# Kernel optimization log

Hardware: AMD Instinct MI355X
Metric: run time of the kernel (lower is better)

Reference implementation:

```python
import jax, jax.numpy as jnp
import numpy as np

MODES1 = 12
MODES2 = 12
IN_CH = 32
OUT_CH = 32
B, H, W = 16, 256, 256
SCALE = 1.0 / (IN_CH * OUT_CH)


def setup_inputs() -> dict:
    key = jax.random.key(0)
    k1, k2, k3 = jax.random.split(key, 3)
    x = jax.random.normal(k1, (B, IN_CH, H, W), dtype=jnp.float32)
    w1 = SCALE * jax.random.uniform(k2, (IN_CH, OUT_CH, MODES1, MODES2, 2), dtype=jnp.float32)
    w2 = SCALE * jax.random.uniform(k3, (IN_CH, OUT_CH, MODES1, MODES2, 2), dtype=jnp.float32)
    return {"x": x, "weights1": w1, "weights2": w2}


def _compl_mul2d(inp, w):
    # inp: [b,i,x,y] complex ; w: [i,o,x,y,2] real -> complex
    wc = jax.lax.complex(w[..., 0], w[..., 1])
    return jnp.einsum('bixy,ioxy->boxy', inp, wc)


def reference(x, weights1, weights2):
    H_, W_ = x.shape[-2], x.shape[-1]
    m1 = min(MODES1, H_ // 2)
    m2 = min(MODES2, W_ // 2 + 1)
    x_ft = jnp.fft.rfft2(x.astype(jnp.float32))  # [B, Cin, H, W//2+1]
    low = _compl_mul2d(x_ft[:, :, :m1, :m2], weights1[:, :, :m1, :m2])
    high = _compl_mul2d(x_ft[:, :, -m1:, :m2], weights2[:, :, :m1, :m2])
    out_ft = jnp.zeros((x.shape[0], OUT_CH, H_, W_ // 2 + 1), dtype=jnp.complex64)
    out_ft = out_ft.at[:, :, :m1, :m2].set(low)
    out_ft = out_ft.at[:, :, H_ - m1:, :m2].set(high)
    return jnp.fft.irfft2(out_ft, s=(H_, W_)).astype(x.dtype)
```

## Files before the change

### kernel.cpp

```cpp
#include <hip/hip_runtime.h>


#define TPI 6.28318530717958647692f

__global__ __launch_bounds__(256, 2) void k12_hwdft(const float* __restrict__ x,
                                                    float* __restrict__ Xf) {
  __shared__ float2 step2[64];
  __shared__ float red[4 * 13 * 128];
  __shared__ float2 Ys2[13 * 130];
  const int blk = blockIdx.x;
  const int bi = blk >> 1, wh = blk & 1;
  const int t = threadIdx.x;
  const int q = t >> 6, l = t & 63;

  if (t < 64) {
    float s, c;
    sincosf(TPI * (float)t * (1.0f / 256.0f), &s, &c);
    step2[t] = make_float2(c, s);
  }
  __syncthreads();

  const float2* xp2 = reinterpret_cast<const float2*>(x + (size_t)bi * 65536 + wh * 128) + l;
  float2 aC[13], aS12[12];
#pragma unroll
  for (int j = 0; j < 13; j++) aC[j] = make_float2(0.f, 0.f);
#pragma unroll
  for (int j = 0; j < 12; j++) aS12[j] = make_float2(0.f, 0.f);

  const int h0 = q * 16;
#pragma unroll 2
  for (int hh = 0; hh < 16; hh++) {
    int h = h0 + hh;
    float2 x0 = xp2[h * 128];
    float2 x1 = xp2[(h + 64) * 128];
    float2 x2 = xp2[(h + 128) * 128];
    float2 x3 = xp2[(h + 192) * 128];
    float2 p02 = make_float2(x0.x + x2.x, x0.y + x2.y);
    float2 m02 = make_float2(x0.x - x2.x, x0.y - x2.y);
    float2 p13 = make_float2(x1.x + x3.x, x1.y + x3.y);
    float2 m13 = make_float2(x1.x - x3.x, x1.y - x3.y);
    float2 A = make_float2(p02.x + p13.x, p02.y + p13.y);
    float2 Bv = make_float2(p02.x - p13.x, p02.y - p13.y);
    aC[0].x += A.x; aC[0].y += A.y;
    float2 st = step2[h];
    float cj = st.x, sj = st.y;
#pragma unroll
    for (int jj = 0; jj < 12; jj++) {
      const int j = jj + 1, r = j & 3;
      if (r == 0) {
        aC[j].x = fmaf(A.x, cj, aC[j].x);   aC[j].y = fmaf(A.y, cj, aC[j].y);
        aS12[jj].x = fmaf(A.x, sj, aS12[jj].x); aS12[jj].y = fmaf(A.y, sj, aS12[jj].y);
      } else if (r == 2) {
        aC[j].x = fmaf(Bv.x, cj, aC[j].x);  aC[j].y = fmaf(Bv.y, cj, aC[j].y);
        aS12[jj].x = fmaf(Bv.x, sj, aS12[jj].x); aS12[jj].y = fmaf(Bv.y, sj, aS12[jj].y);
      } else if (r == 1) {
        aC[j].x = fmaf(m02.x, cj, fmaf(-m13.x, sj, aC[j].x));
        aC[j].y = fmaf(m02.y, cj, fmaf(-m13.y, sj, aC[j].y));
        aS12[jj].x = fmaf(m02.x, sj, fmaf(m13.x, cj, aS12[jj].x));
        aS12[jj].y = fmaf(m02.y, sj, fmaf(m13.y, cj, aS12[jj].y));
      } else {
        aC[j].x = fmaf(m02.x, cj, fmaf(m13.x, sj, aC[j].x));
        aC[j].y = fmaf(m02.y, cj, fmaf(m13.y, sj, aC[j].y));
        aS12[jj].x = fmaf(m02.x, sj, fmaf(-m13.x, cj, aS12[jj].x));
        aS12[jj].y = fmaf(m02.y, sj, fmaf(-m13.y, cj, aS12[jj].y));
      }
      if (jj < 11) {
        float nc = fmaf(cj, st.x, -(sj * st.y));
        float ns = fmaf(cj, st.y, sj * st.x);
        cj = nc; sj = ns;
      }
    }
  }

  for (int p = 0; p < 2; p++) {
    __syncthreads();
#pragma unroll
    for (int cc = 0; cc < 13; cc++) {
      int cls = p * 13 + cc;
      int j = cls >> 1;
      float2 v;
      if (cls & 1) v = (j == 0) ? make_float2(0.f, 0.f) : aS12[j - 1];
      else v = aC[j];
      *reinterpret_cast<float2*>(&red[(q * 13 + cc) * 128 + 2 * l]) = v;
    }
    __syncthreads();
    for (int idx = t; idx < 13 * 128; idx += 256) {
      int cc = idx >> 7, wl = idx & 127;
      int cls = p * 13 + cc;
      float s = red[(0 * 13 + cc) * 128 + wl] + red[(1 * 13 + cc) * 128 + wl] +
                red[(2 * 13 + cc) * 128 + wl] + red[(3 * 13 + cc) * 128 + wl];
      if (cls & 1) Ys2[(cls >> 1) * 130 + wl].y = s;
      else         Ys2[(cls >> 1) * 130 + wl].x = s;
    }
  }
  __syncthreads();

  if (t < 156) {
    int j = t / 12, kx = t % 12;
    float c1, s1, c2, s2;
    {
      float s, c;
      sincosf(TPI * (float)kx * (1.0f / 256.0f), &s, &c);
      c1 = c; s1 = -s;
      sincosf(TPI * (float)((2 * kx) & 255) * (1.0f / 256.0f), &s, &c);
      c2 = c; s2 = -s;
    }
    const float2* CS = &Ys2[j * 130];
    float pr0 = 1.0f, pi0 = 0.0f;
    float pr1 = c1, pi1 = s1;
    float A = 0, B = 0, D = 0, E = 0;
#pragma unroll 4
    for (int w = 0; w < 128; w += 2) {
      float4 vv = *reinterpret_cast<const float4*>(&CS[w]);
      A = fmaf(vv.x, pr0, A); B = fmaf(vv.x, pi0, B);
      D = fmaf(vv.y, pr0, D); E = fmaf(vv.y, pi0, E);
      A = fmaf(vv.z, pr1, A); B = fmaf(vv.z, pi1, B);
      D = fmaf(vv.w, pr1, D); E = fmaf(vv.w, pi1, E);
      float n0r = pr0 * c2 - pi0 * s2, n0i = pr0 * s2 + pi0 * c2;
      float n1r = pr1 * c2 - pi1 * s2, n1i = pr1 * s2 + pi1 * c2;
      pr0 = n0r; pi0 = n0i; pr1 = n1r; pi1 = n1i;
    }
    float sgn = (wh && (kx & 1)) ? -1.0f : 1.0f;
    A *= sgn; B *= sgn; D *= sgn; E *= sgn;
    float2* Xo = reinterpret_cast<float2*>(Xf) + (size_t)wh * 147456;
    size_t base = (size_t)kx * 512 + bi;
    if (j <= 11) Xo[(size_t)j * 6144 + base] = make_float2(A + E, B - D);
    if (j >= 1)  Xo[(size_t)(24 - j) * 6144 + base] = make_float2(A - E, B + D);
  }
}

__global__ __launch_bounds__(256) void k3_mix(const float* __restrict__ Xf,
                                              const float* __restrict__ w1,
                                              const float* __restrict__ w2,
                                              float* __restrict__ Ff) {
  __shared__ float Xs[1024];
  __shared__ float Ws[2048];
  int m = blockIdx.x;
  int ky = m / 12, kx = m % 12;
  int t = threadIdx.x;
  const float* Xsl = Xf + (size_t)m * 1024;
  for (int e = t; e < 1024; e += 256) Xs[e] = Xsl[e] + Xsl[e + 294912];
  const float* Wp = (ky < 12) ? w1 : w2;
  int myr = (ky < 12) ? ky : ky - 12;
  int woff = myr * 24 + kx * 2;
  for (int e = t; e < 1024; e += 256) {
    float2 wv = *reinterpret_cast<const float2*>(Wp + (size_t)e * 288 + woff);
    Ws[e * 2] = wv.x; Ws[e * 2 + 1] = wv.y;
  }
  __syncthreads();
  int o = t & 31, bh = t >> 5;
  float ar = 0, ai = 0, br = 0, bi_ = 0;
#pragma unroll
  for (int i = 0; i < 32; i++) {
    float wr = Ws[i * 64 + o * 2], wi = Ws[i * 64 + o * 2 + 1];
    float x1r = Xs[bh * 64 + i * 2], x1i = Xs[bh * 64 + i * 2 + 1];
    float x2r = Xs[(bh + 8) * 64 + i * 2], x2i = Xs[(bh + 8) * 64 + i * 2 + 1];
    ar = fmaf(x1r, wr, ar); ar = fmaf(-x1i, wi, ar);
    ai = fmaf(x1r, wi, ai); ai = fmaf(x1i, wr, ai);
    br = fmaf(x2r, wr, br); br = fmaf(-x2i, wi, br);
    bi_ = fmaf(x2r, wi, bi_); bi_ = fmaf(x2i, wr, bi_);
  }
  float scale = (kx == 0 ? 1.0f : 2.0f) * (1.0f / 65536.0f);
  float2* Fo = reinterpret_cast<float2*>(Ff) + (size_t)m * 512;
  Fo[(size_t)bh * 32 + o] = make_float2(ar * scale, ai * scale);
  Fo[(size_t)(bh + 8) * 32 + o] = make_float2(br * scale, bi_ * scale);
}

__global__ __launch_bounds__(256) void k45_inv(const float* __restrict__ Ff,
                                               float* __restrict__ out) {
  __shared__ float tw[128 * 27];
  __shared__ float PQ[13 * 12 * 4];
  __shared__ float Gs[256 * 24];
  const int bo = blockIdx.x;
  const int t = threadIdx.x;
  const int l = t & 63, wq = t >> 6;

  for (int e = t; e < 128 * 13; e += 256) {
    int h = e / 13, j = e % 13;
    float s, c;
    sincosf(TPI * (float)((h * j) & 255) * (1.0f / 256.0f), &s, &c);
    tw[h * 27 + 2 * j] = c;
    tw[h * 27 + 2 * j + 1] = s;
  }
  if (t < 156) {
    int j = t / 12, kx = t % 12;
    const float2* F2 = reinterpret_cast<const float2*>(Ff);
    float lr = 0, li = 0, hr = 0, hi = 0;
    if (j < 12) { float2 v = F2[((size_t)j * 12 + kx) * 512 + bo]; lr = v.x; li = v.y; }
    if (j > 0)  { float2 v = F2[((size_t)(24 - j) * 12 + kx) * 512 + bo]; hr = v.x; hi = v.y; }
    PQ[(j * 12 + kx) * 4 + 0] = lr + hr;
    PQ[(j * 12 + kx) * 4 + 1] = li + hi;
    PQ[(j * 12 + kx) * 4 + 2] = hi - li;
    PQ[(j * 12 + kx) * 4 + 3] = lr - hr;
  }
  __syncthreads();

  if (t < 192) {
    const int kx = t % 12, hq = t / 12;
    float Pr[13], Pi[13], Qr[13], Qi[13];
#pragma unroll
    for (int j = 0; j < 13; j++) {
      Pr[j] = PQ[(j * 12 + kx) * 4 + 0];
      Pi[j] = PQ[(j * 12 + kx) * 4 + 1];
      Qr[j] = PQ[(j * 12 + kx) * 4 + 2];
      Qi[j] = PQ[(j * 12 + kx) * 4 + 3];
    }
    for (int hh = 0; hh < 8; hh++) {
      int h = hh * 16 + hq;
      float Er = 0, Ei = 0, Or = 0, Oi = 0;
#pragma unroll
      for (int j = 0; j < 13; j++) {
        float c = tw[h * 27 + 2 * j], s = tw[h * 27 + 2 * j + 1];
        if (j & 1) {
          Or = fmaf(Pr[j], c, Or); Or = fmaf(Qr[j], s, Or);
          Oi = fmaf(Pi[j], c, Oi); Oi = fmaf(Qi[j], s, Oi);
        } else {
          Er = fmaf(Pr[j], c, Er); Er = fmaf(Qr[j], s, Er);
          Ei = fmaf(Pi[j], c, Ei); Ei = fmaf(Qi[j], s, Ei);
        }
      }
      Gs[h * 24 + 2 * kx] = Er + Or;
      Gs[h * 24 + 2 * kx + 1] = Ei + Oi;
      Gs[(h + 128) * 24 + 2 * kx] = Er - Or;
      Gs[(h + 128) * 24 + 2 * kx + 1] = Ei - Oi;
    }
  }

  float cA[12], sA[12], cB[12], sB[12];
#pragma unroll
  for (int kx = 1; kx < 12; kx++) {
    float s, c;
    __sincosf(TPI * (float)((kx * (2 * l)) & 255) * (1.0f / 256.0f), &s, &c);
    cA[kx] = c; sA[kx] = s;
    __sincosf(TPI * (float)((kx * (2 * l + 1)) & 255) * (1.0f / 256.0f), &s, &c);
    cB[kx] = c; sB[kx] = s;
  }
  __syncthreads();

  float* ob0 = out + ((size_t)bo * 256 + wq * 64) * 256;
  for (int rs = 0; rs < 64; rs++) {
    int rl = wq * 64 + rs;
    float g[24];
    const float4* gr4 = reinterpret_cast<const float4*>(&Gs[rl * 24]);
#pragma unroll
    for (int qq = 0; qq < 6; qq++) {
      float4 v = gr4[qq];
      g[4 * qq] = v.x; g[4 * qq + 1] = v.y; g[4 * qq + 2] = v.z; g[4 * qq + 3] = v.w;
    }
    float E0 = g[0], O0 = 0, E1 = g[0], O1 = 0;
#pragma unroll
    for (int kx = 1; kx < 12; kx++) {
      float ta = g[2 * kx] * cA[kx] - g[2 * kx + 1] * sA[kx];
      float tb = g[2 * kx] * cB[kx] - g[2 * kx + 1] * sB[kx];
      if (kx & 1) { O0 += ta; O1 += tb; } else { E0 += ta; E1 += tb; }
    }
    float* orow = ob0 + rs * 256;
    float2 v0 = make_float2(E0 + O0, E1 + O1);
    float2 v1 = make_float2(E0 - O0, E1 - O1);
    __builtin_nontemporal_store(*reinterpret_cast<double*>(&v0),
                                reinterpret_cast<double*>(&orow[2 * l]));
    __builtin_nontemporal_store(*reinterpret_cast<double*>(&v1),
                                reinterpret_cast<double*>(&orow[128 + 2 * l]));
  }
}

extern "C" void kernel_launch(void* const* d_in, const int* in_sizes, int n_in,
                              void* d_out, int out_size, void* d_ws, size_t ws_size,
                              hipStream_t stream) {
  const float* x = (const float*)d_in[0];
  const float* w1 = (const float*)d_in[1];
  const float* w2 = (const float*)d_in[2];
  float* out = (float*)d_out;
  float* ws = (float*)d_ws;

  float* Xf = ws;
  float* Ff = ws + 589824;

  k12_hwdft<<<1024, 256, 0, stream>>>(x, Xf);
  k3_mix<<<288, 256, 0, stream>>>(Xf, w1, w2, Ff);
  k45_inv<<<512, 256, 0, stream>>>(Ff, out);
}
```

Before: 74.98 us.

## Split forward DFT by H-halves instead of W-halves, removing cross-warp reduction

The forward H/W DFT kernel now gives each block half of the H rows across all 256 columns, one column per thread. Previously each block took half the W columns with four warp groups splitting H. This removes the shared-memory reduction stage and its barriers, and the two partial H sums are added later in the mix kernel. It also software-prefetches the next row's four loads and widens the W-direction DFT to 256 points with four twiddle phases. In exchange it uses scalar loads instead of float2, a longer serial H loop per thread, a larger Ys2 buffer, and more sequential work for the 156 threads in the W stage.

```diff
diff --git a/kernel.cpp b/kernel.cpp
--- a/kernel.cpp
+++ b/kernel.cpp
@@ -6,12 +6,10 @@
 __global__ __launch_bounds__(256, 2) void k12_hwdft(const float* __restrict__ x,
                                                     float* __restrict__ Xf) {
   __shared__ float2 step2[64];
-  __shared__ float red[4 * 13 * 128];
-  __shared__ float2 Ys2[13 * 130];
+  __shared__ float2 Ys2[13 * 260];
   const int blk = blockIdx.x;
-  const int bi = blk >> 1, wh = blk & 1;
+  const int bi = blk >> 1, hf = blk & 1;
   const int t = threadIdx.x;
-  const int q = t >> 6, l = t & 63;
 
   if (t < 64) {
     float s, c;
@@ -20,49 +18,47 @@
   }
   __syncthreads();
 
-  const float2* xp2 = reinterpret_cast<const float2*>(x + (size_t)bi * 65536 + wh * 128) + l;
-  float2 aC[13], aS12[12];
-#pragma unroll
-  for (int j = 0; j < 13; j++) aC[j] = make_float2(0.f, 0.f);
-#pragma unroll
-  for (int j = 0; j < 12; j++) aS12[j] = make_float2(0.f, 0.f);
-
-  const int h0 = q * 16;
-#pragma unroll 2
-  for (int hh = 0; hh < 16; hh++) {
+  const float* xp = x + (size_t)bi * 65536 + t;
+  float aC[13], aS12[12];
+#pragma unroll
+  for (int j = 0; j < 13; j++) aC[j] = 0.0f;
+#pragma unroll
+  for (int j = 0; j < 12; j++) aS12[j] = 0.0f;
+
+  const int h0 = hf * 32;
+  float c0 = xp[h0 * 256];
+  float c1 = xp[(h0 + 64) * 256];
+  float c2 = xp[(h0 + 128) * 256];
+  float c3 = xp[(h0 + 192) * 256];
+#pragma unroll 4
+  for (int hh = 0; hh < 32; hh++) {
     int h = h0 + hh;
-    float2 x0 = xp2[h * 128];
-    float2 x1 = xp2[(h + 64) * 128];
-    float2 x2 = xp2[(h + 128) * 128];
-    float2 x3 = xp2[(h + 192) * 128];
-    float2 p02 = make_float2(x0.x + x2.x, x0.y + x2.y);
-    float2 m02 = make_float2(x0.x - x2.x, x0.y - x2.y);
-    float2 p13 = make_float2(x1.x + x3.x, x1.y + x3.y);
-    float2 m13 = make_float2(x1.x - x3.x, x1.y - x3.y);
-    float2 A = make_float2(p02.x + p13.x, p02.y + p13.y);
-    float2 Bv = make_float2(p02.x - p13.x, p02.y - p13.y);
-    aC[0].x += A.x; aC[0].y += A.y;
+    int hn = h0 + ((hh + 1) & 31);
+    float n0 = xp[hn * 256];
+    float n1 = xp[(hn + 64) * 256];
+    float n2 = xp[(hn + 128) * 256];
+    float n3 = xp[(hn + 192) * 256];
+    float p02 = c0 + c2, m02 = c0 - c2;
+    float p13 = c1 + c3, m13 = c1 - c3;
+    float A = p02 + p13, Bv = p02 - p13;
+    aC[0] += A;
     float2 st = step2[h];
     float cj = st.x, sj = st.y;
 #pragma unroll
     for (int jj = 0; jj < 12; jj++) {
       const int j = jj + 1, r = j & 3;
       if (r == 0) {
-        aC[j].x = fmaf(A.x, cj, aC[j].x);   aC[j].y = fmaf(A.y, cj, aC[j].y);
-        aS12[jj].x = fmaf(A.x, sj, aS12[jj].x); aS12[jj].y = fmaf(A.y, sj, aS12[jj].y);
+        aC[j] = fmaf(A, cj, aC[j]);
+        aS12[jj] = fmaf(A, sj, aS12[jj]);
       } else if (r == 2) {
-        aC[j].x = fmaf(Bv.x, cj, aC[j].x);  aC[j].y = fmaf(Bv.y, cj, aC[j].y);
-        aS12[jj].x = fmaf(Bv.x, sj, aS12[jj].x); aS12[jj].y = fmaf(Bv.y, sj, aS12[jj].y);
+        aC[j] = fmaf(Bv, cj, aC[j]);
+        aS12[jj] = fmaf(Bv, sj, aS12[jj]);
       } else if (r == 1) {
-        aC[j].x = fmaf(m02.x, cj, fmaf(-m13.x, sj, aC[j].x));
-        aC[j].y = fmaf(m02.y, cj, fmaf(-m13.y, sj, aC[j].y));
-        aS12[jj].x = fmaf(m02.x, sj, fmaf(m13.x, cj, aS12[jj].x));
-        aS12[jj].y = fmaf(m02.y, sj, fmaf(m13.y, cj, aS12[jj].y));
+        aC[j] = fmaf(m02, cj, fmaf(-m13, sj, aC[j]));
+        aS12[jj] = fmaf(m02, sj, fmaf(m13, cj, aS12[jj]));
       } else {
-        aC[j].x = fmaf(m02.x, cj, fmaf(m13.x, sj, aC[j].x));
-        aC[j].y = fmaf(m02.y, cj, fmaf(m13.y, sj, aC[j].y));
-        aS12[jj].x = fmaf(m02.x, sj, fmaf(-m13.x, cj, aS12[jj].x));
-        aS12[jj].y = fmaf(m02.y, sj, fmaf(-m13.y, cj, aS12[jj].y));
+        aC[j] = fmaf(m02, cj, fmaf(m13, sj, aC[j]));
+        aS12[jj] = fmaf(m02, sj, fmaf(-m13, cj, aS12[jj]));
       }
       if (jj < 11) {
         float nc = fmaf(cj, st.x, -(sj * st.y));
@@ -70,59 +66,47 @@
         cj = nc; sj = ns;
       }
     }
-  }
-
-  for (int p = 0; p < 2; p++) {
-    __syncthreads();
-#pragma unroll
-    for (int cc = 0; cc < 13; cc++) {
-      int cls = p * 13 + cc;
-      int j = cls >> 1;
-      float2 v;
-      if (cls & 1) v = (j == 0) ? make_float2(0.f, 0.f) : aS12[j - 1];
-      else v = aC[j];
-      *reinterpret_cast<float2*>(&red[(q * 13 + cc) * 128 + 2 * l]) = v;
-    }
-    __syncthreads();
-    for (int idx = t; idx < 13 * 128; idx += 256) {
-      int cc = idx >> 7, wl = idx & 127;
-      int cls = p * 13 + cc;
-      float s = red[(0 * 13 + cc) * 128 + wl] + red[(1 * 13 + cc) * 128 + wl] +
-                red[(2 * 13 + cc) * 128 + wl] + red[(3 * 13 + cc) * 128 + wl];
-      if (cls & 1) Ys2[(cls >> 1) * 130 + wl].y = s;
-      else         Ys2[(cls >> 1) * 130 + wl].x = s;
-    }
-  }
+    c0 = n0; c1 = n1; c2 = n2; c3 = n3;
+  }
+
+#pragma unroll
+  for (int j = 0; j < 13; j++)
+    Ys2[j * 260 + t] = make_float2(aC[j], (j == 0) ? 0.0f : aS12[j - 1]);
   __syncthreads();
 
   if (t < 156) {
     int j = t / 12, kx = t % 12;
-    float c1, s1, c2, s2;
+    float p1r, p1i, p2r, p2i, p3r, p3i, c4, s4;
     {
       float s, c;
-      sincosf(TPI * (float)kx * (1.0f / 256.0f), &s, &c);
-      c1 = c; s1 = -s;
-      sincosf(TPI * (float)((2 * kx) & 255) * (1.0f / 256.0f), &s, &c);
-      c2 = c; s2 = -s;
-    }
-    const float2* CS = &Ys2[j * 130];
-    float pr0 = 1.0f, pi0 = 0.0f;
-    float pr1 = c1, pi1 = s1;
+      sincosf(TPI * (float)kx * (1.0f / 256.0f), &s, &c);          p1r = c; p1i = -s;
+      sincosf(TPI * (float)((2 * kx) & 255) * (1.0f / 256.0f), &s, &c); p2r = c; p2i = -s;
+      sincosf(TPI * (float)((3 * kx) & 255) * (1.0f / 256.0f), &s, &c); p3r = c; p3i = -s;
+      sincosf(TPI * (float)((4 * kx) & 255) * (1.0f / 256.0f), &s, &c); c4 = c; s4 = -s;
+    }
+    const float2* CS = &Ys2[j * 260];
+    float p0r = 1.0f, p0i = 0.0f;
     float A = 0, B = 0, D = 0, E = 0;
 #pragma unroll 4
-    for (int w = 0; w < 128; w += 2) {
-      float4 vv = *reinterpret_cast<const float4*>(&CS[w]);
-      A = fmaf(vv.x, pr0, A); B = fmaf(vv.x, pi0, B);
-      D = fmaf(vv.y, pr0, D); E = fmaf(vv.y, pi0, E);
-      A = fmaf(vv.z, pr1, A); B = fmaf(vv.z, pi1, B);
-      D = fmaf(vv.w, pr1, D); E = fmaf(vv.w, pi1, E);
-      float n0r = pr0 * c2 - pi0 * s2, n0i = pr0 * s2 + pi0 * c2;
-      float n1r = pr1 * c2 - pi1 * s2, n1i = pr1 * s2 + pi1 * c2;
-      pr0 = n0r; pi0 = n0i; pr1 = n1r; pi1 = n1i;
-    }
-    float sgn = (wh && (kx & 1)) ? -1.0f : 1.0f;
-    A *= sgn; B *= sgn; D *= sgn; E *= sgn;
-    float2* Xo = reinterpret_cast<float2*>(Xf) + (size_t)wh * 147456;
+    for (int w = 0; w < 256; w += 4) {
+      float4 v01 = *reinterpret_cast<const float4*>(&CS[w]);
+      float4 v23 = *reinterpret_cast<const float4*>(&CS[w + 2]);
+      A = fmaf(v01.x, p0r, A); B = fmaf(v01.x, p0i, B);
+      D = fmaf(v01.y, p0r, D); E = fmaf(v01.y, p0i, E);
+      A = fmaf(v01.z, p1r, A); B = fmaf(v01.z, p1i, B);
+      D = fmaf(v01.w, p1r, D); E = fmaf(v01.w, p1i, E);
+      A = fmaf(v23.x, p2r, A); B = fmaf(v23.x, p2i, B);
+      D = fmaf(v23.y, p2r, D); E = fmaf(v23.y, p2i, E);
+      A = fmaf(v23.z, p3r, A); B = fmaf(v23.z, p3i, B);
+      D = fmaf(v23.w, p3r, D); E = fmaf(v23.w, p3i, E);
+      float r0 = p0r * c4 - p0i * s4, i0 = p0r * s4 + p0i * c4;
+      float r1 = p1r * c4 - p1i * s4, i1 = p1r * s4 + p1i * c4;
+      float r2 = p2r * c4 - p2i * s4, i2 = p2r * s4 + p2i * c4;
+      float r3 = p3r * c4 - p3i * s4, i3 = p3r * s4 + p3i * c4;
+      p0r = r0; p0i = i0; p1r = r1; p1i = i1;
+      p2r = r2; p2i = i2; p3r = r3; p3i = i3;
+    }
+    float2* Xo = reinterpret_cast<float2*>(Xf) + (size_t)hf * 147456;
     size_t base = (size_t)kx * 512 + bi;
     if (j <= 11) Xo[(size_t)j * 6144 + base] = make_float2(A + E, B - D);
     if (j >= 1)  Xo[(size_t)(24 - j) * 6144 + base] = make_float2(A - E, B + D);
```

Result: slower. 78.80 us (+5.1%).
